# Kernel optimization log

Hardware: AMD Instinct MI355X
Metric: run time of the kernel (lower is better)

## Reference

```python
import jax, jax.numpy as jnp
import numpy as np

N_EMBD = 1024
HEAD_SIZE = 64
BATCH = 4
T = 4096  # == block_size


def setup_inputs() -> dict:
    key = jax.random.key(0)
    kx, kq, kk, kv = jax.random.split(key, 4)
    x = jax.random.normal(kx, (BATCH, T, N_EMBD), dtype=jnp.float32)
    Wq = jax.random.normal(kq, (N_EMBD, HEAD_SIZE), dtype=jnp.float32) * 0.02
    Wk = jax.random.normal(kk, (N_EMBD, HEAD_SIZE), dtype=jnp.float32) * 0.02
    Wv = jax.random.normal(kv, (N_EMBD, HEAD_SIZE), dtype=jnp.float32) * 0.02
    return {"x": x, "Wq": Wq, "Wk": Wk, "Wv": Wv}


def reference(x, Wq, Wk, Wv):
    # x: [B, T, C]; projections: [B, T, H]
    B, Tlen, C = x.shape
    q = jnp.einsum('btc,ch->bth', x, Wq)
    k = jnp.einsum('btc,ch->bth', x, Wk)
    v = jnp.einsum('btc,ch->bth', x, Wv)
    # NOTE: original scales by C**-0.5 where C = n_embd (input channels), not head_size
    scale = jnp.asarray(C, x.dtype) ** -0.5
    wei = jnp.einsum('bth,bsh->bts', q, k) * scale  # [B, T, T]
    causal = jnp.tril(jnp.ones((Tlen, Tlen), dtype=bool))
    wei = jnp.where(causal, wei, -jnp.inf)
    wei = jax.nn.softmax(wei, axis=-1)
    # dropout p=0.0 -> identity
    out = jnp.einsum('bts,bsh->bth', wei, v)  # [B, T, H]
    return out
```

## Files before the change

### kernel.cpp

```cpp
#include <hip/hip_runtime.h>
#include <math.h>

#define T_SEQ 4096
#define NBATCH 4
#define NEMBD 1024
#define HS 64
#define BT (NBATCH * T_SEQ)

typedef float f32x4 __attribute__((ext_vector_type(4)));
typedef short s8v  __attribute__((ext_vector_type(8)));
typedef short s4v  __attribute__((ext_vector_type(4)));

__device__ __forceinline__ short f2b_rne(float f) {
    union { float f; unsigned u; } v; v.f = f;
    unsigned r = v.u + 0x7fffu + ((v.u >> 16) & 1u);
    return (short)(r >> 16);
}
__device__ __forceinline__ unsigned pk2(float lo, float hi) {
    return __builtin_amdgcn_perm(__float_as_uint(hi), __float_as_uint(lo), 0x07060302u);
}

__global__ __launch_bounds__(256) void wtrans_kernel(
        const float* __restrict__ Wq, const float* __restrict__ Wk,
        const float* __restrict__ Wv, short* __restrict__ Wt) {
    int e = blockIdx.x * 256 + threadIdx.x;
    int col = e & 63, k = (e >> 6) & 1023, mat = e >> 16;
    const float* W = (mat == 0) ? Wq : ((mat == 1) ? Wk : Wv);
    float scale = (mat == 0) ? 0.0450842298f : 1.0f;
    Wt[(size_t)(mat * 64 + col) * 1024 + k] = f2b_rne(W[k * 64 + col] * scale);
}

__global__ __launch_bounds__(256) void proj_kernel(
        const float* __restrict__ x, const short* __restrict__ Wt,
        short* __restrict__ QKV) {
    int tid = threadIdx.x;
    int w = tid >> 6, l = tid & 63, quad = l >> 4, c16 = l & 15;
    int row0 = blockIdx.x * 32;
    short* VpT = QKV + 2 * (size_t)BT * HS;

    const float* xr0 = x + (size_t)(row0 + c16) * NEMBD;
    const float* xr1 = x + (size_t)(row0 + 16 + c16) * NEMBD;
    const short* wp  = Wt + (size_t)(w * 48 + c16) * 1024;

    f32x4 acc[2][3] = {};
    for (int ko = 0; ko < NEMBD; ko += 32) {
        int off = ko + quad * 8;
        union { s8v v; unsigned u[4]; } a0, a1;
        float4 p0 = *(const float4*)(xr0 + off), p1 = *(const float4*)(xr0 + off + 4);
        a0.u[0] = pk2(p0.x, p0.y); a0.u[1] = pk2(p0.z, p0.w);
        a0.u[2] = pk2(p1.x, p1.y); a0.u[3] = pk2(p1.z, p1.w);
        float4 r0 = *(const float4*)(xr1 + off), r1 = *(const float4*)(xr1 + off + 4);
        a1.u[0] = pk2(r0.x, r0.y); a1.u[1] = pk2(r0.z, r0.w);
        a1.u[2] = pk2(r1.x, r1.y); a1.u[3] = pk2(r1.z, r1.w);
        s8v b0 = *(const s8v*)(wp + off);
        s8v b1 = *(const s8v*)(wp + 16 * 1024 + off);
        s8v b2 = *(const s8v*)(wp + 32 * 1024 + off);
        acc[0][0] = __builtin_amdgcn_mfma_f32_16x16x32_bf16(a0.v, b0, acc[0][0], 0, 0, 0);
        acc[0][1] = __builtin_amdgcn_mfma_f32_16x16x32_bf16(a0.v, b1, acc[0][1], 0, 0, 0);
        acc[0][2] = __builtin_amdgcn_mfma_f32_16x16x32_bf16(a0.v, b2, acc[0][2], 0, 0, 0);
        acc[1][0] = __builtin_amdgcn_mfma_f32_16x16x32_bf16(a1.v, b0, acc[1][0], 0, 0, 0);
        acc[1][1] = __builtin_amdgcn_mfma_f32_16x16x32_bf16(a1.v, b1, acc[1][1], 0, 0, 0);
        acc[1][2] = __builtin_amdgcn_mfma_f32_16x16x32_bf16(a1.v, b2, acc[1][2], 0, 0, 0);
    }
    #pragma unroll
    for (int rg = 0; rg < 2; rg++)
        #pragma unroll
        for (int j = 0; j < 3; j++) {
            int g = w * 48 + j * 16 + c16;
            int mat = g >> 6, h = g & 63;
            if (mat < 2) {
                #pragma unroll
                for (int r = 0; r < 4; r++) {
                    int row = row0 + rg * 16 + quad * 4 + r;
                    QKV[(size_t)mat * BT * HS + (size_t)row * HS + h] = f2b_rne(acc[rg][j][r]);
                }
            } else {
                s4v pv;
                #pragma unroll
                for (int r = 0; r < 4; r++) pv[r] = f2b_rne(acc[rg][j][r]);
                *(s4v*)(VpT + (size_t)h * BT + row0 + rg * 16 + quad * 4) = pv;
            }
        }
}

__global__ __launch_bounds__(512, 4) void attn_kernel(
        const short* __restrict__ QKV, float* __restrict__ out) {
    __shared__ float smem[9216];
    short* Ps = (short*)smem;

    int tid = threadIdx.x;
    int w = tid >> 6, l = tid & 63, quad = l >> 4, c16 = l & 15;
    int bi = blockIdx.x;
    int b  = bi & 3;
    int jt = 127 - (bi >> 2);
    int q0 = jt * 32;

    const short* Qp  = QKV;
    const short* Kp  = QKV + (size_t)BT * HS;
    const short* VpT = QKV + 2 * (size_t)BT * HS;
    size_t bT = (size_t)b * T_SEQ;

    s8v qf[2][2];
    #pragma unroll
    for (int qt = 0; qt < 2; qt++)
        #pragma unroll
        for (int h = 0; h < 2; h++)
            qf[qt][h] = *(const s8v*)(Qp + (bT + q0 + qt * 16 + c16) * HS + h * 32 + quad * 8);

    f32x4 o[2][4] = {};
    float lsum[2] = {0.f, 0.f};
    int nkt = (q0 >> 6) + 1;
    short* Pw[2] = { Ps + (w * 2) * 1152, Ps + (w * 2 + 1) * 1152 };

    for (int kt = w; kt < nkt; kt += 8) {
        int kb = kt * 64;
        bool last = (kt == nkt - 1);
        f32x4 st[2][4];
        #pragma unroll
        for (int nt = 0; nt < 4; nt++) {
            const short* kr = Kp + (bT + kb + nt * 16 + c16) * HS + quad * 8;
            s8v k0 = *(const s8v*)kr;
            s8v k1 = *(const s8v*)(kr + 32);
            f32x4 z0 = {0.f, 0.f, 0.f, 0.f}, z1 = {0.f, 0.f, 0.f, 0.f};
            z0 = __builtin_amdgcn_mfma_f32_16x16x32_bf16(k0, qf[0][0], z0, 0, 0, 0);
            z0 = __builtin_amdgcn_mfma_f32_16x16x32_bf16(k1, qf[0][1], z0, 0, 0, 0);
            z1 = __builtin_amdgcn_mfma_f32_16x16x32_bf16(k0, qf[1][0], z1, 0, 0, 0);
            z1 = __builtin_amdgcn_mfma_f32_16x16x32_bf16(k1, qf[1][1], z1, 0, 0, 0);
            st[0][nt] = z0; st[1][nt] = z1;
        }
        #pragma unroll
        for (int qt = 0; qt < 2; qt++) {
            int qrow = q0 + qt * 16 + c16;
            #pragma unroll
            for (int nt = 0; nt < 4; nt++) {
                float p[4];
                #pragma unroll
                for (int r = 0; r < 4; r++) {
                    float v = st[qt][nt][r];
                    if (last && (kb + nt * 16 + quad * 4 + r > qrow)) v = -30000.f;
                    p[r] = __builtin_amdgcn_exp2f(v);
                    lsum[qt] += p[r];
                }
                union { s4v v; unsigned u[2]; } pkv;
                pkv.u[0] = pk2(p[0], p[1]); pkv.u[1] = pk2(p[2], p[3]);
                *(s4v*)(Pw[qt] + c16 * 72 + nt * 16 + quad * 4) = pkv.v;
            }
        }
        s8v pa[2][2];
        #pragma unroll
        for (int qt = 0; qt < 2; qt++) {
            pa[qt][0] = *(const s8v*)(Pw[qt] + c16 * 72 + quad * 8);
            pa[qt][1] = *(const s8v*)(Pw[qt] + c16 * 72 + quad * 8 + 32);
        }
        #pragma unroll
        for (int nt = 0; nt < 4; nt++) {
            const short* vr = VpT + (size_t)(nt * 16 + c16) * BT + bT + kb + quad * 8;
            s8v v0 = *(const s8v*)vr;
            s8v v1 = *(const s8v*)(vr + 32);
            #pragma unroll
            for (int qt = 0; qt < 2; qt++) {
                o[qt][nt] = __builtin_amdgcn_mfma_f32_16x16x32_bf16(pa[qt][0], v0, o[qt][nt], 0, 0, 0);
                o[qt][nt] = __builtin_amdgcn_mfma_f32_16x16x32_bf16(pa[qt][1], v1, o[qt][nt], 0, 0, 0);
            }
        }
    }

    #pragma unroll
    for (int qt = 0; qt < 2; qt++) {
        lsum[qt] += __shfl_xor(lsum[qt], 16);
        lsum[qt] += __shfl_xor(lsum[qt], 32);
    }

    #pragma unroll
    for (int qt = 0; qt < 2; qt++) {
        __syncthreads();
        #pragma unroll
        for (int nt = 0; nt < 4; nt++)
            *(f32x4*)(smem + ((w * 4 + nt) * 64 + l) * 4) = o[qt][nt];
        if (l < 16) smem[8192 + w * 16 + l] = lsum[qt];
        __syncthreads();
        if (w < 4) {
            f32x4 os = {0.f, 0.f, 0.f, 0.f}, ls = {0.f, 0.f, 0.f, 0.f};
            #pragma unroll
            for (int s = 0; s < 8; s++) {
                os += *(const f32x4*)(smem + ((s * 4 + w) * 64 + l) * 4);
                ls += *(const f32x4*)(smem + 8192 + s * 16 + quad * 4);
            }
            #pragma unroll
            for (int r = 0; r < 4; r++)
                out[(bT + q0 + qt * 16 + quad * 4 + r) * HS + w * 16 + c16] = os[r] / ls[r];
        }
    }
}

extern "C" void kernel_launch(void* const* d_in, const int* in_sizes, int n_in,
                              void* d_out, int out_size, void* d_ws, size_t ws_size,
                              hipStream_t stream) {
    const float* x  = (const float*)d_in[0];
    const float* Wq = (const float*)d_in[1];
    const float* Wk = (const float*)d_in[2];
    const float* Wv = (const float*)d_in[3];
    float* out = (float*)d_out;

    short* QKV = (short*)d_ws;
    short* Wt  = QKV + (size_t)3 * BT * HS;

    wtrans_kernel<<<768, 256, 0, stream>>>(Wq, Wk, Wv, Wt);
    proj_kernel<<<BT / 32, 256, 0, stream>>>(x, Wt, QKV);
    attn_kernel<<<512, 512, 0, stream>>>(QKV, out);
}
```

Baseline: 187.4 us.

## Stage x tiles through shared memory in projection with 512-thread blocks

The projection kernel now runs 8 waves per block instead of 4. The waves cooperatively load a 32x64 fp32 slice of x once, convert it to bf16 and store it in LDS, while the next slice is prefetched into registers. Each wave then computes one 16-row tile against 48 output columns, so its accumulator state drops from 6 to 3 MFMA tiles. This targets coalescing and parallelism of the x reads, but adds two block barriers per 64-wide k step, and W is still read directly from global memory by every wave.

```diff
diff --git a/kernel.cpp b/kernel.cpp
--- a/kernel.cpp
+++ b/kernel.cpp
@@ -30,57 +30,62 @@
     Wt[(size_t)(mat * 64 + col) * 1024 + k] = f2b_rne(W[k * 64 + col] * scale);
 }
 
-__global__ __launch_bounds__(256) void proj_kernel(
+__global__ __launch_bounds__(512, 4) void proj_kernel(
         const float* __restrict__ x, const short* __restrict__ Wt,
         short* __restrict__ QKV) {
+    __shared__ short xs[32 * 72];
     int tid = threadIdx.x;
     int w = tid >> 6, l = tid & 63, quad = l >> 4, c16 = l & 15;
+    int rt = w >> 2, ws = w & 3;
     int row0 = blockIdx.x * 32;
     short* VpT = QKV + 2 * (size_t)BT * HS;
 
-    const float* xr0 = x + (size_t)(row0 + c16) * NEMBD;
-    const float* xr1 = x + (size_t)(row0 + 16 + c16) * NEMBD;
-    const short* wp  = Wt + (size_t)(w * 48 + c16) * 1024;
-
-    f32x4 acc[2][3] = {};
-    for (int ko = 0; ko < NEMBD; ko += 32) {
-        int off = ko + quad * 8;
-        union { s8v v; unsigned u[4]; } a0, a1;
-        float4 p0 = *(const float4*)(xr0 + off), p1 = *(const float4*)(xr0 + off + 4);
-        a0.u[0] = pk2(p0.x, p0.y); a0.u[1] = pk2(p0.z, p0.w);
-        a0.u[2] = pk2(p1.x, p1.y); a0.u[3] = pk2(p1.z, p1.w);
-        float4 r0 = *(const float4*)(xr1 + off), r1 = *(const float4*)(xr1 + off + 4);
-        a1.u[0] = pk2(r0.x, r0.y); a1.u[1] = pk2(r0.z, r0.w);
-        a1.u[2] = pk2(r1.x, r1.y); a1.u[3] = pk2(r1.z, r1.w);
-        s8v b0 = *(const s8v*)(wp + off);
-        s8v b1 = *(const s8v*)(wp + 16 * 1024 + off);
-        s8v b2 = *(const s8v*)(wp + 32 * 1024 + off);
-        acc[0][0] = __builtin_amdgcn_mfma_f32_16x16x32_bf16(a0.v, b0, acc[0][0], 0, 0, 0);
-        acc[0][1] = __builtin_amdgcn_mfma_f32_16x16x32_bf16(a0.v, b1, acc[0][1], 0, 0, 0);
-        acc[0][2] = __builtin_amdgcn_mfma_f32_16x16x32_bf16(a0.v, b2, acc[0][2], 0, 0, 0);
-        acc[1][0] = __builtin_amdgcn_mfma_f32_16x16x32_bf16(a1.v, b0, acc[1][0], 0, 0, 0);
-        acc[1][1] = __builtin_amdgcn_mfma_f32_16x16x32_bf16(a1.v, b1, acc[1][1], 0, 0, 0);
-        acc[1][2] = __builtin_amdgcn_mfma_f32_16x16x32_bf16(a1.v, b2, acc[1][2], 0, 0, 0);
-    }
-    #pragma unroll
-    for (int rg = 0; rg < 2; rg++)
-        #pragma unroll
-        for (int j = 0; j < 3; j++) {
-            int g = w * 48 + j * 16 + c16;
-            int mat = g >> 6, h = g & 63;
-            if (mat < 2) {
-                #pragma unroll
-                for (int r = 0; r < 4; r++) {
-                    int row = row0 + rg * 16 + quad * 4 + r;
-                    QKV[(size_t)mat * BT * HS + (size_t)row * HS + h] = f2b_rne(acc[rg][j][r]);
-                }
-            } else {
-                s4v pv;
-                #pragma unroll
-                for (int r = 0; r < 4; r++) pv[r] = f2b_rne(acc[rg][j][r]);
-                *(s4v*)(VpT + (size_t)h * BT + row0 + rg * 16 + quad * 4) = pv;
-            }
-        }
+    int srow = tid >> 4, skc = (tid & 15) * 4;
+    const float* gx = x + (size_t)(row0 + srow) * NEMBD + skc;
+    const short* wp = Wt + (size_t)(ws * 48 + c16) * 1024;
+
+    float4 pf = *(const float4*)gx;
+    f32x4 acc[3] = {};
+
+    for (int ko = 0; ko < NEMBD; ko += 64) {
+        {
+            union { s4v v; unsigned u[2]; } pkv;
+            pkv.u[0] = pk2(pf.x, pf.y); pkv.u[1] = pk2(pf.z, pf.w);
+            *(s4v*)(xs + srow * 72 + skc) = pkv.v;
+        }
+        __syncthreads();
+        {
+            int kn = (ko + 64 < NEMBD) ? (ko + 64) : 0;
+            pf = *(const float4*)(gx + kn);
+        }
+        #pragma unroll
+        for (int ks = 0; ks < 2; ks++) {
+            s8v a = *(const s8v*)(xs + (rt * 16 + c16) * 72 + ks * 32 + quad * 8);
+            #pragma unroll
+            for (int j = 0; j < 3; j++) {
+                s8v b = *(const s8v*)(wp + (size_t)j * 16 * 1024 + ko + ks * 32 + quad * 8);
+                acc[j] = __builtin_amdgcn_mfma_f32_16x16x32_bf16(a, b, acc[j], 0, 0, 0);
+            }
+        }
+        __syncthreads();
+    }
+    #pragma unroll
+    for (int j = 0; j < 3; j++) {
+        int g = ws * 48 + j * 16 + c16;
+        int mat = g >> 6, h = g & 63;
+        if (mat < 2) {
+            #pragma unroll
+            for (int r = 0; r < 4; r++) {
+                int row = row0 + rt * 16 + quad * 4 + r;
+                QKV[(size_t)mat * BT * HS + (size_t)row * HS + h] = f2b_rne(acc[j][r]);
+            }
+        } else {
+            s4v pv;
+            #pragma unroll
+            for (int r = 0; r < 4; r++) pv[r] = f2b_rne(acc[j][r]);
+            *(s4v*)(VpT + (size_t)h * BT + row0 + rt * 16 + quad * 4) = pv;
+        }
+    }
 }
 
 __global__ __launch_bounds__(512, 4) void attn_kernel(
@@ -206,6 +211,6 @@
     short* Wt  = QKV + (size_t)3 * BT * HS;
 
     wtrans_kernel<<<768, 256, 0, stream>>>(Wq, Wk, Wv, Wt);
-    proj_kernel<<<BT / 32, 256, 0, stream>>>(x, Wt, QKV);
+    proj_kernel<<<BT / 32, 512, 0, stream>>>(x, Wt, QKV);
     attn_kernel<<<512, 512, 0, stream>>>(QKV, out);
 }
```

Measured after the change: 185.5 us. Within noise of the previous version (-1.0%).
